# Optimization experiments

Measured on AMD Instinct MI355X. Metric: run time of the kernel, lower is better.

The kernel has to match this reference:

```python
import jax, jax.numpy as jnp
import numpy as np
from jax import lax

B, NH, NW, C, H = 8, 32, 32, 384, 12
N = NH * NW
HD = C // H
HID = 2 * C
SCALE = HD ** -0.5
EPS = 1e-5


def _rel_index(nh, nw):
    coords = np.stack(np.meshgrid(np.arange(nh), np.arange(nw), indexing='ij'))  # [2,nh,nw]
    cf = coords.reshape(2, -1)                      # [2, N]
    rel = (cf[:, :, None] - cf[:, None, :]).transpose(1, 2, 0).astype(np.int64)  # [N,N,2]
    rel[:, :, 0] += nh - 1
    rel[:, :, 1] += nw - 1
    rel[:, :, 0] *= 2 * nw - 1
    return jnp.asarray(rel.sum(-1), dtype=jnp.int32)  # [N,N]


def setup_inputs() -> dict:
    key = jax.random.key(0)
    ks = jax.random.split(key, 10)
    nrel = (2 * NH - 1) * (2 * NW - 1)
    return {
        'x': jax.random.normal(ks[0], (B, N, C), jnp.float32),
        'n_h': NH,
        'n_w': NW,
        'rel_index': _rel_index(NH, NW),
        'ln1_g': jnp.ones((C,), jnp.float32),
        'ln1_b': jnp.zeros((C,), jnp.float32),
        'w_qkv': jax.random.normal(ks[1], (3 * C, C), jnp.float32) * 0.02,
        'w_proj': jax.random.normal(ks[2], (C, C), jnp.float32) * 0.02,
        'b_proj': jnp.zeros((C,), jnp.float32),
        'rel_table': jax.random.normal(ks[3], (nrel, H), jnp.float32) * 0.02,
        'global_bias': jax.random.normal(ks[4], (max(N, 1024), max(N, 1024)), jnp.float32) * 0.02,
        'ln2_g': jnp.ones((C,), jnp.float32),
        'ln2_b': jnp.zeros((C,), jnp.float32),
        'w_pw1': jax.random.normal(ks[5], (HID, C, 1, 1), jnp.float32) * 0.05,
        'b_pw1': jnp.zeros((HID,), jnp.float32),
        'w_dw': jax.random.normal(ks[6], (HID, 1, 3, 3), jnp.float32) * 0.05,
        'b_dw': jnp.zeros((HID,), jnp.float32),
        'w_pw2': jax.random.normal(ks[7], (C, HID, 1, 1), jnp.float32) * 0.05,
        'b_pw2': jnp.zeros((C,), jnp.float32),
    }


def _layernorm(x, g, b):
    m = jnp.mean(x, axis=-1, keepdims=True)
    v = jnp.mean((x - m) ** 2, axis=-1, keepdims=True)
    return (x - m) * lax.rsqrt(v + EPS) * g + b


def _conv(x, w, b, pad, dil, groups):
    y = lax.conv_general_dilated(x, w, window_strides=(1, 1),
                                 padding=[(pad, pad), (pad, pad)],
                                 rhs_dilation=(dil, dil),
                                 dimension_numbers=('NCHW', 'OIHW', 'NCHW'),
                                 feature_group_count=groups)
    return y + b[None, :, None, None]


def _mlp(x, n_h, n_w, w_pw1, b_pw1, w_dw, b_dw, w_pw2, b_pw2):
    b, n, c = x.shape
    fmap = x.transpose(0, 2, 1).reshape(b, c, n_h, n_w)          # tokens -> map
    y = _conv(fmap, w_pw1, b_pw1, 0, 1, 1)                       # 1x1
    y = jax.nn.gelu(y, approximate=False)
    y = _conv(y, w_dw, b_dw, 2, 2, HID)                          # depthwise dilated 3x3
    y = jax.nn.gelu(y, approximate=False)
    y = _conv(y, w_pw2, b_pw2, 0, 1, 1)                          # 1x1
    return y.reshape(b, c, n).transpose(0, 2, 1)                 # map -> tokens


def _attn(x, rel_index, w_qkv, w_proj, b_proj, rel_table, global_bias):
    b, n, c = x.shape
    qkv = (x @ w_qkv.T).reshape(b, n, 3, H, HD).transpose(2, 0, 3, 1, 4)  # [3,B,H,N,HD]
    q, k, v = qkv[0], qkv[1], qkv[2]
    scores = jnp.einsum('bhqd,bhkd->bhqk', q, k) * SCALE
    rpb = rel_table[rel_index].transpose(2, 0, 1)                # [H,N,N]
    gb = global_bias[:n, :n]                                     # [N,N]
    scores = scores + rpb[None] + gb[None, None]
    attn = jax.nn.softmax(scores, axis=-1)
    out = jnp.einsum('bhqk,bhkd->bhqd', attn, v).transpose(0, 2, 1, 3).reshape(b, n, c)
    return out @ w_proj.T + b_proj


def reference(x, n_h, n_w, rel_index, ln1_g, ln1_b, w_qkv, w_proj, b_proj,
              rel_table, global_bias, ln2_g, ln2_b,
              w_pw1, b_pw1, w_dw, b_dw, w_pw2, b_pw2):
    # forward order in source: MLP block first, then attention block
    x = x + _mlp(_layernorm(x, ln2_g, ln2_b), n_h, n_w, w_pw1, b_pw1, w_dw, b_dw, w_pw2, b_pw2)
    x = x + _attn(_layernorm(x, ln1_g, ln1_b), rel_index, w_qkv, w_proj, b_proj, rel_table, global_bias)
    return x
```

## Files before the change

kernel.cpp:

```cpp
#include <hip/hip_runtime.h>
#include <cstdint>
#include <cstddef>

using ushort_t = unsigned short;

#define DEVI __device__ __forceinline__

typedef __attribute__((ext_vector_type(8))) __bf16 bf16x8;
typedef __attribute__((ext_vector_type(4))) float f32x4;
typedef __attribute__((ext_vector_type(8))) unsigned short u16x8;
typedef __attribute__((ext_vector_type(4))) unsigned short u16x4;

DEVI ushort_t f2bf(float f) {
  unsigned u = __builtin_bit_cast(unsigned, f);
  u += 0x7FFFu + ((u >> 16) & 1u);
  return (ushort_t)(u >> 16);
}
DEVI float bf2f(ushort_t h) {
  unsigned u = ((unsigned)h) << 16;
  return __builtin_bit_cast(float, u);
}
DEVI bf16x8 ldb8(const ushort_t* p) {
  return __builtin_bit_cast(bf16x8, *(const u16x8*)p);
}
DEVI float geluf(float x) { return 0.5f * x * (1.0f + erff(x * 0.70710678118654752f)); }

DEVI void gload16(const void* g, void* l) {
  __builtin_amdgcn_global_load_lds((const __attribute__((address_space(1))) void*)g,
                                   (__attribute__((address_space(3))) void*)l, 16, 0, 0);
}
#if __has_builtin(__builtin_amdgcn_exp2f)
DEVI float exp2a(float x) { return __builtin_amdgcn_exp2f(x); }
#else
DEVI float exp2a(float x) {
  float r;
  asm("v_exp_f32 %0, %1" : "=v"(r) : "v"(x));
  return r;
}
#endif

#define LOG2E 1.4426950408889634f
#define SCALE_QL 0.2550348281f

__global__ __launch_bounds__(256) void convert_k(
    const float* __restrict__ wqkv, const float* __restrict__ wproj,
    const float* __restrict__ wpw1, const float* __restrict__ wpw2,
    const float* __restrict__ wdw,
    ushort_t* __restrict__ o_qkv, ushort_t* __restrict__ o_proj,
    ushort_t* __restrict__ o_pw1, ushort_t* __restrict__ o_pw2,
    ushort_t* __restrict__ o_dwt) {
  int i = blockIdx.x * 256 + threadIdx.x;
  if (i < 442368) { o_qkv[i] = f2bf(wqkv[i]); return; }
  i -= 442368;
  if (i < 147456) { o_proj[i] = f2bf(wproj[i]); return; }
  i -= 147456;
  if (i < 294912) { o_pw1[i] = f2bf(wpw1[i]); return; }
  i -= 294912;
  if (i < 294912) { o_pw2[i] = f2bf(wpw2[i]); return; }
  i -= 294912;
  const int c = i / 9, tap = i % 9;
  o_dwt[tap * 768 + c] = f2bf(wdw[i]);
}

__global__ __launch_bounds__(256) void ln_k(const float* __restrict__ x,
                                            const float* __restrict__ g,
                                            const float* __restrict__ bta,
                                            ushort_t* __restrict__ out) {
  const int w = threadIdx.x >> 6, l = threadIdx.x & 63;
  const size_t row = (size_t)blockIdx.x * 4 + w;
  const float* xr = x + row * 384;
  float v[6];
  float s = 0.f;
#pragma unroll
  for (int i = 0; i < 6; i++) { v[i] = xr[i * 64 + l]; s += v[i]; }
#pragma unroll
  for (int off = 32; off; off >>= 1) s += __shfl_xor(s, off);
  const float mean = s * (1.0f / 384.0f);
  float q2 = 0.f;
#pragma unroll
  for (int i = 0; i < 6; i++) { const float d = v[i] - mean; q2 += d * d; }
#pragma unroll
  for (int off = 32; off; off >>= 1) q2 += __shfl_xor(q2, off);
  const float rstd = rsqrtf(q2 * (1.0f / 384.0f) + 1e-5f);
  ushort_t* orow = out + row * 384;
#pragma unroll
  for (int i = 0; i < 6; i++) {
    const int c = i * 64 + l;
    orow[c] = f2bf((v[i] - mean) * rstd * g[c] + bta[c]);
  }
}

__global__ __launch_bounds__(256) void dwconv_k(const ushort_t* __restrict__ y1,
                                                const ushort_t* __restrict__ wdwt,
                                                const float* __restrict__ bdw,
                                                ushort_t* __restrict__ y2) {
  const int tid = blockIdx.x * 256 + threadIdx.x;
  const int cg = tid % 96;
  const int pix = (tid / 96) & 1023;
  const int b_ = tid / (96 * 1024);
  const int hh = pix >> 5, ww = pix & 31;
  const int c0 = cg * 8;
  float acc[8];
#pragma unroll
  for (int j = 0; j < 8; j++) acc[j] = bdw[c0 + j];
#pragma unroll
  for (int kh = 0; kh < 3; kh++) {
    const int h2 = hh + 2 * kh - 2;
    if ((unsigned)h2 >= 32u) continue;
#pragma unroll
    for (int kw = 0; kw < 3; kw++) {
      const int w2 = ww + 2 * kw - 2;
      if ((unsigned)w2 >= 32u) continue;
      const u16x8 iv = *(const u16x8*)&y1[((size_t)(b_ << 10) + (h2 << 5) + w2) * 768 + c0];
      const u16x8 wv = *(const u16x8*)&wdwt[(kh * 3 + kw) * 768 + c0];
#pragma unroll
      for (int j = 0; j < 8; j++) acc[j] += bf2f(iv[j]) * bf2f(wv[j]);
    }
  }
  u16x8 ov;
#pragma unroll
  for (int j = 0; j < 8; j++) ov[j] = f2bf(geluf(acc[j]));
  *(u16x8*)&y2[((size_t)(b_ << 10) + pix) * 768 + c0] = ov;
}

__global__ __launch_bounds__(256) void biaspre_k(const int* __restrict__ ridx,
                                                 const float* __restrict__ rtab,
                                                 const float* __restrict__ gb,
                                                 ushort_t* __restrict__ biasf) {
  const int lin = blockIdx.x * 256 + threadIdx.x;
  const int l = lin & 63, k16 = (lin >> 6) & 63, q16 = lin >> 12;
  const int lg = l >> 4, lr = l & 15;
  const int q = q16 * 16 + lr, k0 = k16 * 16 + lg * 4;
  const int4 iv = *(const int4*)&ridx[q * 1024 + k0];
  const float4 gv = *(const float4*)&gb[q * 1024 + k0];
  const int idx[4] = {iv.x, iv.y, iv.z, iv.w};
  const float g4[4] = {gv.x, gv.y, gv.z, gv.w};
  float rv[4][12];
#pragma unroll
  for (int r = 0; r < 4; r++) {
    const float4 t0 = *(const float4*)&rtab[idx[r] * 12];
    const float4 t1 = *(const float4*)&rtab[idx[r] * 12 + 4];
    const float4 t2 = *(const float4*)&rtab[idx[r] * 12 + 8];
    rv[r][0] = t0.x; rv[r][1] = t0.y; rv[r][2] = t0.z; rv[r][3] = t0.w;
    rv[r][4] = t1.x; rv[r][5] = t1.y; rv[r][6] = t1.z; rv[r][7] = t1.w;
    rv[r][8] = t2.x; rv[r][9] = t2.y; rv[r][10] = t2.z; rv[r][11] = t2.w;
  }
#pragma unroll
  for (int h = 0; h < 12; h++) {
    u16x4 ov;
#pragma unroll
    for (int r = 0; r < 4; r++) ov[r] = f2bf((rv[r][h] + g4[r]) * LOG2E);
    *(u16x4*)&biasf[(((size_t)(h * 64 + q16) * 64 + k16) * 64 + l) * 4] = ov;
  }
}

template <int BM, int BN, int MR, int NR, int EPI>
__global__ __launch_bounds__(256) void gemm_k(
    const ushort_t* __restrict__ A, const ushort_t* __restrict__ Bw, int K, int Ncols,
    const float* __restrict__ bias, const float* __restrict__ resid,
    void* __restrict__ o0, void* __restrict__ o1, void* __restrict__ o2) {
  constexpr int WN = BN / (16 * NR);
  constexpr int WM = BM / (16 * MR);
  static_assert(WM * WN == 4, "4 waves");
  constexpr int ABUF = BM * 64, BUFSZ = (BM + BN) * 64;
  constexpr int AUNITS = BM * 8, BUNITS = BN * 8;
  __shared__ ushort_t smem[2 * BUFSZ];
  const int tid = threadIdx.x, w = tid >> 6, l = tid & 63;
  const int lg = l >> 4, lr = l & 15;
  constexpr int MT = 8192 / BM;
  const int mt = blockIdx.x % MT, nt = blockIdx.x / MT;
  const int trow = mt * BM, tcol = nt * BN;
  const int wr = w / WN, wc = w % WN;

  f32x4 acc[MR][NR];
#pragma unroll
  for (int m = 0; m < MR; m++)
#pragma unroll
    for (int n = 0; n < NR; n++) acc[m][n] = (f32x4){0.f, 0.f, 0.f, 0.f};

  auto stage = [&](int buf, int k0) {
    ushort_t* sb = &smem[buf * BUFSZ];
#pragma unroll
    for (int u0 = 0; u0 < AUNITS; u0 += 256) {
      const int u = u0 + tid;
      const int row = u >> 3, s = u & 7;
      gload16(A + (size_t)(trow + row) * K + k0 + ((s ^ (row & 7)) << 3),
              sb + (u0 + w * 64) * 8);
    }
    ushort_t* sbB = sb + ABUF;
#pragma unroll
    for (int u0 = 0; u0 < BUNITS; u0 += 256) {
      const int u = u0 + tid;
      const int row = u >> 3, s = u & 7;
      gload16(Bw + (size_t)(tcol + row) * K + k0 + ((s ^ (row & 7)) << 3),
              sbB + (u0 + w * 64) * 8);
    }
  };

  const int nsteps = K >> 6;
  stage(0, 0);
  __syncthreads();
  for (int t = 0; t < nsteps; t++) {
    if (t + 1 < nsteps) stage((t + 1) & 1, (t + 1) << 6);
    const int bo = (t & 1) * BUFSZ;
    bf16x8 af[2][MR], bfr[2][NR];
#pragma unroll
    for (int kk = 0; kk < 2; kk++) {
#pragma unroll
      for (int m = 0; m < MR; m++) {
        const int ra = wr * (MR * 16) + m * 16 + lr;
        af[kk][m] = ldb8(&smem[bo + ra * 64 + (((kk * 4 + lg) ^ (ra & 7)) << 3)]);
      }
#pragma unroll
      for (int n = 0; n < NR; n++) {
        const int rb = wc * (NR * 16) + n * 16 + lr;
        bfr[kk][n] = ldb8(&smem[bo + ABUF + rb * 64 + (((kk * 4 + lg) ^ (rb & 7)) << 3)]);
      }
    }
#pragma unroll
    for (int kk = 0; kk < 2; kk++)
#pragma unroll
      for (int m = 0; m < MR; m++)
#pragma unroll
        for (int n = 0; n < NR; n++)
          acc[m][n] =
              __builtin_amdgcn_mfma_f32_16x16x32_bf16(af[kk][m], bfr[kk][n], acc[m][n], 0, 0, 0);
    __syncthreads();
  }

#pragma unroll
  for (int m = 0; m < MR; m++) {
    const int rowb = trow + wr * (MR * 16) + m * 16 + lg * 4;
#pragma unroll
    for (int n = 0; n < NR; n++) {
      const int col = tcol + wc * (NR * 16) + n * 16 + lr;
#pragma unroll
      for (int r = 0; r < 4; r++) {
        const float v = acc[m][n][r];
        const int rw = rowb + r;
        if constexpr (EPI == 0) {
          ((ushort_t*)o0)[(size_t)rw * Ncols + col] = f2bf(geluf(v + bias[col]));
        } else if constexpr (EPI == 1) {
          ((float*)o0)[(size_t)rw * 384 + col] =
              resid[(size_t)rw * 384 + col] + v + bias[col];
        } else {
          const int sel = col / 384, c2 = col % 384, hh = c2 >> 5, d = c2 & 31;
          const int b_ = rw >> 10, nn = rw & 1023;
          const size_t bh = (size_t)(b_ * 12 + hh);
          if (sel == 0) {
            ((ushort_t*)o0)[(bh * 1024 + nn) * 32 + d] = f2bf(v * SCALE_QL);
          } else if (sel == 1) {
            ((ushort_t*)o1)[(bh * 1024 + nn) * 32 + (d & 7) +
                            (((d >> 3) ^ ((nn >> 1) & 3)) << 3)] = f2bf(v);
          } else {
            const int kt = nn >> 6, rem = nn & 63, p = rem >> 5, ks = rem & 31;
            const int lgv = (ks & 15) >> 2, jv = ((ks >> 4) << 2) | (ks & 3);
            const int dh = d >> 4, lrv = d & 15;
            ((ushort_t*)o2)[bh * 32768 + kt * 2048 + (p * 2 + dh) * 512 +
                            (lgv * 16 + lrv) * 8 + jv] = f2bf(v);
          }
        }
      }
    }
  }
}

__global__ __launch_bounds__(256) void attn_k(const ushort_t* __restrict__ Q,
                                              const ushort_t* __restrict__ Kb,
                                              const ushort_t* __restrict__ Vt,
                                              const ushort_t* __restrict__ biasf,
                                              ushort_t* __restrict__ AO) {
  __shared__ ushort_t smem[8192];
  const int tid = threadIdx.x, w = tid >> 6, l = tid & 63, lg = l >> 4, lr = l & 15;
  const int L = (blockIdx.x & 7) * 96 + (blockIdx.x >> 3);
  const int h = L >> 6, rem = L & 63, b_ = rem >> 3, qb = rem & 7;
  const int q16A = qb * 8 + w, q16B = q16A + 4;
  const int qrow0A = q16A << 4, qrow0B = q16B << 4;
  const size_t bh = (size_t)(b_ * 12 + h);
  const ushort_t* kb = Kb + bh * 32768;
  const ushort_t* vbf = Vt + bh * 32768;
  const ushort_t* bbA = biasf + (size_t)(h * 64 + q16A) * 16384 + l * 4;
  const ushort_t* bbB = biasf + (size_t)(h * 64 + q16B) * 16384 + l * 4;
  const bf16x8 qfA = ldb8(Q + (bh * 1024 + qrow0A + lr) * 32 + lg * 8);
  const bf16x8 qfB = ldb8(Q + (bh * 1024 + qrow0B + lr) * 32 + lg * 8);
  u16x8 onesu;
#pragma unroll
  for (int j = 0; j < 8; j++) onesu[j] = 0x3F80;
  const bf16x8 onesf = __builtin_bit_cast(bf16x8, onesu);

  auto stage = [&](int buf, int kt) {
    ushort_t* base = &smem[buf * 4096];
    gload16(kb + (kt << 6) * 32 + w * 512 + l * 8, base + w * 512);
    gload16(vbf + kt * 2048 + w * 512 + l * 8, base + 2048 + w * 512);
  };

  f32x4 oA0 = {0.f, 0.f, 0.f, 0.f}, oA1 = oA0, oB0 = oA0, oB1 = oA0;
  f32x4 oSA = oA0, oSB = oA0;

  stage(0, 0);
  asm volatile("s_waitcnt vmcnt(0)");
  __syncthreads();

  for (int kt = 0; kt < 16; kt++) {
    const int buf = kt & 1;
    if (kt < 15) stage(buf ^ 1, kt + 1);
    u16x4 b4A[4], b4B[4];
#pragma unroll
    for (int kf = 0; kf < 4; kf++) {
      b4A[kf] = *(const u16x4*)(bbA + (size_t)(kt * 4 + kf) * 256);
      b4B[kf] = *(const u16x4*)(bbB + (size_t)(kt * 4 + kf) * 256);
    }
    const ushort_t* base = &smem[buf * 4096];
    bf16x8 kfr[4];
#pragma unroll
    for (int kf = 0; kf < 4; kf++)
      kfr[kf] = ldb8(base + (kf * 16 + lr) * 32 + ((lg ^ ((lr >> 1) & 3)) << 3));
    bf16x8 vfr[4];
#pragma unroll
    for (int dv = 0; dv < 4; dv++) vfr[dv] = ldb8(base + 2048 + dv * 512 + l * 8);
    f32x4 sA[4], sB[4];
#pragma unroll
    for (int kf = 0; kf < 4; kf++) {
      f32x4 cA, cB;
#pragma unroll
      for (int r = 0; r < 4; r++) { cA[r] = bf2f(b4A[kf][r]); cB[r] = bf2f(b4B[kf][r]); }
      sA[kf] = __builtin_amdgcn_mfma_f32_16x16x32_bf16(kfr[kf], qfA, cA, 0, 0, 0);
      sB[kf] = __builtin_amdgcn_mfma_f32_16x16x32_bf16(kfr[kf], qfB, cB, 0, 0, 0);
    }
#pragma unroll
    for (int kf = 0; kf < 4; kf++)
#pragma unroll
      for (int r = 0; r < 4; r++) {
        sA[kf][r] = exp2a(sA[kf][r]);
        sB[kf][r] = exp2a(sB[kf][r]);
      }
#pragma unroll
    for (int p = 0; p < 2; p++) {
      bf16x8 paA, paB;
#pragma unroll
      for (int j = 0; j < 4; j++) {
        paA[j] = (__bf16)sA[2 * p][j];
        paA[4 + j] = (__bf16)sA[2 * p + 1][j];
        paB[j] = (__bf16)sB[2 * p][j];
        paB[4 + j] = (__bf16)sB[2 * p + 1][j];
      }
      oA0 = __builtin_amdgcn_mfma_f32_16x16x32_bf16(paA, vfr[p * 2 + 0], oA0, 0, 0, 0);
      oA1 = __builtin_amdgcn_mfma_f32_16x16x32_bf16(paA, vfr[p * 2 + 1], oA1, 0, 0, 0);
      oSA = __builtin_amdgcn_mfma_f32_16x16x32_bf16(paA, onesf, oSA, 0, 0, 0);
      oB0 = __builtin_amdgcn_mfma_f32_16x16x32_bf16(paB, vfr[p * 2 + 0], oB0, 0, 0, 0);
      oB1 = __builtin_amdgcn_mfma_f32_16x16x32_bf16(paB, vfr[p * 2 + 1], oB1, 0, 0, 0);
      oSB = __builtin_amdgcn_mfma_f32_16x16x32_bf16(paB, onesf, oSB, 0, 0, 0);
    }
    if (kt < 15) {
      asm volatile("s_waitcnt vmcnt(0)");
      __syncthreads();
    }
  }
#pragma unroll
  for (int r = 0; r < 4; r++) {
    const float liA = 1.0f / oSA[r];
    const float liB = 1.0f / oSB[r];
    const size_t rowA = ((size_t)(b_ << 10) + qrow0A + lg * 4 + r) * 384 + h * 32;
    const size_t rowB = ((size_t)(b_ << 10) + qrow0B + lg * 4 + r) * 384 + h * 32;
    AO[rowA + lr] = f2bf(oA0[r] * liA);
    AO[rowA + 16 + lr] = f2bf(oA1[r] * liA);
    AO[rowB + lr] = f2bf(oB0[r] * liB);
    AO[rowB + 16 + lr] = f2bf(oB1[r] * liB);
  }
}

constexpr size_t WS_WQKV = 0;
constexpr size_t WS_WPROJ = WS_WQKV + 884736;
constexpr size_t WS_WPW1 = WS_WPROJ + 294912;
constexpr size_t WS_WPW2 = WS_WPW1 + 589824;
constexpr size_t WS_WDWT = WS_WPW2 + 589824;
constexpr size_t WS_XLN = WS_WDWT + 16384;
constexpr size_t WS_Y1 = WS_XLN + 6291456;
constexpr size_t WS_Y2 = WS_Y1 + 12582912;
constexpr size_t WS_X1 = WS_Y2 + 12582912;
constexpr size_t WS_Q = WS_X1 + 12582912;
constexpr size_t WS_K = WS_Q + 6291456;
constexpr size_t WS_VT = WS_K + 6291456;
constexpr size_t WS_BIAS = WS_VT + 6291456;
constexpr size_t WS_AO = WS_BIAS + 25165824;

extern "C" void kernel_launch(void* const* d_in, const int* in_sizes, int n_in,
                              void* d_out, int out_size, void* d_ws, size_t ws_size,
                              hipStream_t stream) {
  (void)in_sizes; (void)n_in; (void)out_size; (void)ws_size;
  const float* x = (const float*)d_in[0];
  const int* rel_index = (const int*)d_in[3];
  const float* ln1_g = (const float*)d_in[4];
  const float* ln1_b = (const float*)d_in[5];
  const float* w_qkv = (const float*)d_in[6];
  const float* w_proj = (const float*)d_in[7];
  const float* b_proj = (const float*)d_in[8];
  const float* rel_table = (const float*)d_in[9];
  const float* gbias = (const float*)d_in[10];
  const float* ln2_g = (const float*)d_in[11];
  const float* ln2_b = (const float*)d_in[12];
  const float* w_pw1 = (const float*)d_in[13];
  const float* b_pw1 = (const float*)d_in[14];
  const float* w_dw = (const float*)d_in[15];
  const float* b_dw = (const float*)d_in[16];
  const float* w_pw2 = (const float*)d_in[17];
  const float* b_pw2 = (const float*)d_in[18];
  float* out = (float*)d_out;

  char* ws = (char*)d_ws;
  ushort_t* wq_bf = (ushort_t*)(ws + WS_WQKV);
  ushort_t* wp_bf = (ushort_t*)(ws + WS_WPROJ);
  ushort_t* w1_bf = (ushort_t*)(ws + WS_WPW1);
  ushort_t* w2_bf = (ushort_t*)(ws + WS_WPW2);
  ushort_t* wdwt = (ushort_t*)(ws + WS_WDWT);
  ushort_t* xln = (ushort_t*)(ws + WS_XLN);
  ushort_t* y1 = (ushort_t*)(ws + WS_Y1);
  ushort_t* y2 = (ushort_t*)(ws + WS_Y2);
  float* x1f = (float*)(ws + WS_X1);
  ushort_t* qb = (ushort_t*)(ws + WS_Q);
  ushort_t* kbuf = (ushort_t*)(ws + WS_K);
  ushort_t* vtb = (ushort_t*)(ws + WS_VT);
  ushort_t* biasf = (ushort_t*)(ws + WS_BIAS);
  ushort_t* ao = (ushort_t*)(ws + WS_AO);

  convert_k<<<4635, 256, 0, stream>>>(w_qkv, w_proj, w_pw1, w_pw2, w_dw,
                                      wq_bf, wp_bf, w1_bf, w2_bf, wdwt);
  biaspre_k<<<1024, 256, 0, stream>>>(rel_index, rel_table, gbias, biasf);

  ln_k<<<2048, 256, 0, stream>>>(x, ln2_g, ln2_b, xln);
  gemm_k<128, 64, 4, 2, 0><<<768, 256, 0, stream>>>(xln, w1_bf, 384, 768, b_pw1,
                                                    nullptr, y1, nullptr, nullptr);
  dwconv_k<<<3072, 256, 0, stream>>>(y1, wdwt, b_dw, y2);
  gemm_k<64, 64, 2, 2, 1><<<768, 256, 0, stream>>>(y2, w2_bf, 768, 384, b_pw2, x,
                                                   x1f, nullptr, nullptr);

  ln_k<<<2048, 256, 0, stream>>>(x1f, ln1_g, ln1_b, xln);
  gemm_k<128, 64, 4, 2, 2><<<1152, 256, 0, stream>>>(xln, wq_bf, 384, 1152, nullptr,
                                                     nullptr, qb, kbuf, vtb);
  attn_k<<<768, 256, 0, stream>>>(qb, kbuf, vtb, biasf, ao);
  gemm_k<64, 64, 2, 2, 1><<<768, 256, 0, stream>>>(ao, wp_bf, 384, 384, b_proj, x1f,
                                                   out, nullptr, nullptr);
}
```

Measured before the change: 214.3 us.

## Triple-buffer LDS staging in GEMM and attention with one barrier per step

Moves the GEMM and attention kernels from double to triple-buffered LDS staging. Each step waits with a partial vmcnt and a single s_barrier, replacing the two __syncthreads per step, so loads two steps ahead overlap the MFMA work. The pw1 and QKV GEMMs also switch to 64x64 tiles with twice as many blocks. The extra LDS per block may lower occupancy, and the smaller tiles reload operands more often.

After: 215.0 us. No clear change (+0.3%).

```diff
diff --git a/kernel.cpp b/kernel.cpp
--- a/kernel.cpp
+++ b/kernel.cpp
@@ -164,7 +164,8 @@
   static_assert(WM * WN == 4, "4 waves");
   constexpr int ABUF = BM * 64, BUFSZ = (BM + BN) * 64;
   constexpr int AUNITS = BM * 8, BUNITS = BN * 8;
-  __shared__ ushort_t smem[2 * BUFSZ];
+  constexpr int SLOADS = AUNITS / 256 + BUNITS / 256;
+  __shared__ ushort_t smem[3 * BUFSZ];
   const int tid = threadIdx.x, w = tid >> 6, l = tid & 63;
   const int lg = l >> 4, lr = l & 15;
   constexpr int MT = 8192 / BM;
@@ -199,10 +200,16 @@
 
   const int nsteps = K >> 6;
   stage(0, 0);
-  __syncthreads();
+  stage(1, 64);
+  int cur = 0;
   for (int t = 0; t < nsteps; t++) {
-    if (t + 1 < nsteps) stage((t + 1) & 1, (t + 1) << 6);
-    const int bo = (t & 1) * BUFSZ;
+    if (t == nsteps - 1)
+      asm volatile("s_waitcnt vmcnt(0)" ::: "memory");
+    else
+      asm volatile("s_waitcnt vmcnt(%0)" ::"i"(SLOADS) : "memory");
+    __builtin_amdgcn_s_barrier();
+    if (t + 2 < nsteps) stage(cur == 0 ? 2 : cur - 1, (t + 2) << 6);
+    const int bo = cur * BUFSZ;
     bf16x8 af[2][MR], bfr[2][NR];
 #pragma unroll
     for (int kk = 0; kk < 2; kk++) {
@@ -225,7 +232,7 @@
         for (int n = 0; n < NR; n++)
           acc[m][n] =
               __builtin_amdgcn_mfma_f32_16x16x32_bf16(af[kk][m], bfr[kk][n], acc[m][n], 0, 0, 0);
-    __syncthreads();
+    cur = (cur == 2) ? 0 : cur + 1;
   }
 
 #pragma unroll
@@ -270,7 +277,7 @@
                                               const ushort_t* __restrict__ Vt,
                                               const ushort_t* __restrict__ biasf,
                                               ushort_t* __restrict__ AO) {
-  __shared__ ushort_t smem[8192];
+  __shared__ ushort_t smem[12288];
   const int tid = threadIdx.x, w = tid >> 6, l = tid & 63, lg = l >> 4, lr = l & 15;
   const int L = (blockIdx.x & 7) * 96 + (blockIdx.x >> 3);
   const int h = L >> 6, rem = L & 63, b_ = rem >> 3, qb = rem & 7;
@@ -298,19 +305,23 @@
   f32x4 oSA = oA0, oSB = oA0;
 
   stage(0, 0);
-  asm volatile("s_waitcnt vmcnt(0)");
-  __syncthreads();
-
+  stage(1, 1);
+  int cur = 0;
   for (int kt = 0; kt < 16; kt++) {
-    const int buf = kt & 1;
-    if (kt < 15) stage(buf ^ 1, kt + 1);
+    if (kt == 15)
+      asm volatile("s_waitcnt vmcnt(0)" ::: "memory");
+    else
+      asm volatile("s_waitcnt vmcnt(2)" ::: "memory");
+    __builtin_amdgcn_s_barrier();
     u16x4 b4A[4], b4B[4];
 #pragma unroll
     for (int kf = 0; kf < 4; kf++) {
       b4A[kf] = *(const u16x4*)(bbA + (size_t)(kt * 4 + kf) * 256);
       b4B[kf] = *(const u16x4*)(bbB + (size_t)(kt * 4 + kf) * 256);
     }
-    const ushort_t* base = &smem[buf * 4096];
+    __builtin_amdgcn_sched_barrier(0);
+    if (kt + 2 < 16) stage(cur == 0 ? 2 : cur - 1, kt + 2);
+    const ushort_t* base = &smem[cur * 4096];
     bf16x8 kfr[4];
 #pragma unroll
     for (int kf = 0; kf < 4; kf++)
@@ -351,10 +362,7 @@
       oB1 = __builtin_amdgcn_mfma_f32_16x16x32_bf16(paB, vfr[p * 2 + 1], oB1, 0, 0, 0);
       oSB = __builtin_amdgcn_mfma_f32_16x16x32_bf16(paB, onesf, oSB, 0, 0, 0);
     }
-    if (kt < 15) {
-      asm volatile("s_waitcnt vmcnt(0)");
-      __syncthreads();
-    }
+    cur = (cur == 2) ? 0 : cur + 1;
   }
 #pragma unroll
   for (int r = 0; r < 4; r++) {
@@ -428,15 +436,15 @@
   biaspre_k<<<1024, 256, 0, stream>>>(rel_index, rel_table, gbias, biasf);
 
   ln_k<<<2048, 256, 0, stream>>>(x, ln2_g, ln2_b, xln);
-  gemm_k<128, 64, 4, 2, 0><<<768, 256, 0, stream>>>(xln, w1_bf, 384, 768, b_pw1,
+  gemm_k<64, 64, 2, 2, 0><<<1536, 256, 0, stream>>>(xln, w1_bf, 384, 768, b_pw1,
                                                     nullptr, y1, nullptr, nullptr);
   dwconv_k<<<3072, 256, 0, stream>>>(y1, wdwt, b_dw, y2);
   gemm_k<64, 64, 2, 2, 1><<<768, 256, 0, stream>>>(y2, w2_bf, 768, 384, b_pw2, x,
                                                    x1f, nullptr, nullptr);
 
   ln_k<<<2048, 256, 0, stream>>>(x1f, ln1_g, ln1_b, xln);
-  gemm_k<128, 64, 4, 2, 2><<<1152, 256, 0, stream>>>(xln, wq_bf, 384, 1152, nullptr,
-                                                     nullptr, qb, kbuf, vtb);
+  gemm_k<64, 64, 2, 2, 2><<<2304, 256, 0, stream>>>(xln, wq_bf, 384, 1152, nullptr,
+                                                    nullptr, qb, kbuf, vtb);
   attn_k<<<768, 256, 0, stream>>>(qb, kbuf, vtb, biasf, ao);
   gemm_k<64, 64, 2, 2, 1><<<768, 256, 0, stream>>>(ao, wp_bf, 384, 384, b_proj, x1f,
                                                    out, nullptr, nullptr);
```
